# Performance work log

Hardware: AMD Instinct MI355X
Metric: run time of the kernel (lower is better)

The kernel has to match this reference:

```python
import jax, jax.numpy as jnp
import numpy as np

N_NODES = 8192
N_EDGES = 65536
D_MODEL = 64
D_INNER = 128
D_STATE = 16
DT_RANK = 4
LAYER_NUM = 3
TAU = 0.01


def _unif(key, shape, fan_out):
    stdv = 1.0 / np.sqrt(fan_out)
    return jax.random.uniform(key, shape, jnp.float32, -stdv, stdv)


def setup_inputs() -> dict:
    key = jax.random.key(0)
    ks = jax.random.split(key, 12)
    x = jax.random.normal(ks[0], (N_NODES, D_MODEL), jnp.float32)
    edge_index = jax.random.randint(ks[1], (2, N_EDGES), 0, N_NODES, jnp.int64)
    in_proj_w = _unif(ks[2], (D_MODEL, 2 * D_INNER), 2 * D_INNER)
    x_proj_w = _unif(ks[3], (D_INNER, DT_RANK + 2 * D_STATE), DT_RANK + 2 * D_STATE)
    dt_proj_w = _unif(ks[4], (DT_RANK, D_INNER), D_INNER)
    out_proj_w = _unif(ks[5], (D_INNER, D_MODEL), D_MODEL)
    A_log = jnp.log(jnp.broadcast_to(jnp.arange(1, D_STATE + 1, dtype=jnp.float32)[None, :], (D_INNER, D_STATE)))
    D = jnp.ones((D_INNER,), jnp.float32)
    in_act_w = _unif(ks[6], (D_INNER, 2), 2)
    in_act_b = _unif(ks[7], (2,), 2)
    out_act_w = _unif(ks[8], (D_INNER, 2), 2)
    out_act_b = _unif(ks[9], (2,), 2)
    return {"x": x, "in_proj_w": in_proj_w, "x_proj_w": x_proj_w, "dt_proj_w": dt_proj_w,
            "A_log": A_log, "D": D, "out_proj_w": out_proj_w,
            "in_act_w": in_act_w, "in_act_b": in_act_b, "out_act_w": out_act_w, "out_act_b": out_act_b,
            "edge_index": edge_index, "layer_num": LAYER_NUM}


def _norm_adj(row, col, w, n_nodes):
    # SparseTensor(...).set_diag() adds diag value 1; symmetric deg^-1/2 renorm
    deg = jax.ops.segment_sum(w, row, num_segments=n_nodes) + 1.0
    dinv = jnp.where(deg > 0, deg ** -0.5, 0.0)
    return dinv[row] * w * dinv[col], dinv * dinv  # off-diag edge weights, diag weights


def _spmm(row, col, ew, dw, x, n_nodes):
    # adj @ x with adj = edges(ew) + diag(dw); x: [N, F]
    return jax.ops.segment_sum(ew[:, None] * x[col], row, num_segments=n_nodes) + dw[:, None] * x


def _gumbel_hard(logits, key, tau):
    g = jax.random.gumbel(key, logits.shape, logits.dtype)
    y = jax.nn.softmax((logits + g) / tau, axis=-1)
    hard = jax.nn.one_hot(jnp.argmax(y, axis=-1), logits.shape[-1], dtype=y.dtype)
    return hard + y - jax.lax.stop_gradient(y)


def reference(x, in_proj_w, x_proj_w, dt_proj_w, A_log, D, out_proj_w,
              in_act_w, in_act_b, out_act_w, out_act_b, edge_index, layer_num):
    n_nodes, d_model = x.shape
    d_inner = dt_proj_w.shape[1]
    n = A_log.shape[1]
    dt_rank = dt_proj_w.shape[0]
    row, col = edge_index[0], edge_index[1]

    xl = jnp.broadcast_to(x[:, None, :], (n_nodes, layer_num, d_model))  # [N,L,d_model]
    x_and_res = xl @ in_proj_w                                           # [N,L,2*d_inner]
    xs, res = jnp.split(x_and_res, 2, axis=-1)
    xs = jax.nn.relu(xs)                                                 # u in scan

    A = -jnp.exp(A_log)                                                  # [d_inner, n]
    x_dbl = xs @ x_proj_w                                                # [N,L,dt_rank+2n]
    delta = jax.nn.softplus(x_dbl[..., :dt_rank] @ dt_proj_w)            # [N,L,d_inner]
    B = x_dbl[..., dt_rank:dt_rank + n]                                  # [N,L,n]
    C = x_dbl[..., dt_rank + n:]                                         # [N,L,n]

    deltaA = jnp.exp(jnp.einsum('bld,dn->bldn', delta, A))               # [N,L,d_inner,n]
    deltaB_u = jnp.einsum('bld,bln->bldn', delta * xs, B)                # [N,L,d_inner,n]

    # initial adjacency: unit-weight edges, sym-normalized with self loops
    ew, dw = _norm_adj(row, col, jnp.ones((row.shape[0],), xs.dtype), n_nodes)
    state = jnp.zeros((n_nodes, d_inner, n), xs.dtype)
    gkey = jax.random.key(42)
    ys = []
    for i in range(layer_num):  # small fixed number of GCN/SSM steps
        state = deltaA[:, i] * state + deltaB_u[:, i]
        y = jnp.einsum('bdn,bn->bd', state, C[:, i])                     # [N,d_inner]
        flat = _spmm(row, col, ew, dw, state.reshape(n_nodes, d_inner * n), n_nodes)
        state = flat.reshape(n_nodes, d_inner, n)
        in_p = _gumbel_hard(y @ in_act_w + in_act_b, jax.random.fold_in(gkey, 2 * i), TAU)
        out_p = _gumbel_hard(y @ out_act_w + out_act_b, jax.random.fold_in(gkey, 2 * i + 1), TAU)
        w = in_p[col, 0] * out_p[row, 0]  # keep_in_prob[v] * keep_out_prob[u]
        ew, dw = _norm_adj(row, col, w, n_nodes)
        ys.append(y)

    y = jnp.stack(ys, axis=1) + xs * D                                   # [N,L,d_inner]
    y = y * jax.nn.relu(res)
    out = y @ out_proj_w                                                 # [N,L,d_model]
    return out[:, -1, :]
```

## Files before the change

kernel.cpp:

```cpp
#include <hip/hip_runtime.h>
#include <cstdint>

#define NN 8192
#define NE 65536
#define G 8
#define CAP 64

typedef _Float16 h8 __attribute__((ext_vector_type(8)));
typedef _Float16 h2 __attribute__((ext_vector_type(2)));

__device__ inline int rdlane_i(int v, int l) {
  return __builtin_amdgcn_readlane(v, l);
}
__device__ inline float rdlane_f(float v, int l) {
  return __int_as_float(__builtin_amdgcn_readlane(__float_as_int(v), l));
}

__host__ __device__ inline void tf2x32(uint32_t k0, uint32_t k1,
                                       uint32_t x0, uint32_t x1,
                                       uint32_t& r0, uint32_t& r1) {
  uint32_t ks2 = k0 ^ k1 ^ 0x1BD11BDAu;
  x0 += k0; x1 += k1;
#define TF_ROT(x,d) (((x)<<(d))|((x)>>(32-(d))))
#define TF_R4(ra,rb,rc,rd) \
  x0+=x1; x1=TF_ROT(x1,ra); x1^=x0; \
  x0+=x1; x1=TF_ROT(x1,rb); x1^=x0; \
  x0+=x1; x1=TF_ROT(x1,rc); x1^=x0; \
  x0+=x1; x1=TF_ROT(x1,rd); x1^=x0;
  TF_R4(13,15,26,6)  x0+=k1;  x1+=ks2+1u;
  TF_R4(17,29,16,24) x0+=ks2; x1+=k0+2u;
  TF_R4(13,15,26,6)  x0+=k0;  x1+=k1+3u;
  TF_R4(17,29,16,24) x0+=k1;  x1+=ks2+4u;
  TF_R4(13,15,26,6)  x0+=ks2; x1+=k0+5u;
  r0=x0; r1=x1;
#undef TF_R4
#undef TF_ROT
}

__device__ inline float gumbel32(uint32_t k0, uint32_t k1, uint32_t idx) {
  uint32_t a, b;
  tf2x32(k0, k1, 0u, idx, a, b);
  uint32_t bits = a ^ b;
  float f = __uint_as_float((bits >> 9) | 0x3f800000u) - 1.0f;
  float u = (f > 0.0f) ? f : 1.17549435e-38f;
  return -logf(-logf(u));
}

__global__ __launch_bounds__(256) void k_nodeprep(
    const float* __restrict__ x, const float* __restrict__ ipw,
    const float* __restrict__ xpw, const float* __restrict__ dtw,
    const float* __restrict__ iaw, const float* __restrict__ iab,
    const float* __restrict__ oaw, const float* __restrict__ oab,
    const float* __restrict__ alog, const float* __restrict__ wout,
    const int* __restrict__ ei,
    uint32_t ki0, uint32_t ki1, uint32_t ko0, uint32_t ko1,
    float* __restrict__ xs, float* __restrict__ rres,
    float* __restrict__ delta, _Float16* __restrict__ dxh2,
    float* __restrict__ Bm, float* __restrict__ Cm,
    float* __restrict__ inp, float* __restrict__ outp,
    float* __restrict__ Amat, _Float16* __restrict__ woT,
    int* __restrict__ cnt, int* __restrict__ csr_col) {
  __shared__ float sxs[G][128];
  __shared__ float sdbl[G][36];
  __shared__ float sdx[G][128];
  int t = threadIdx.x;
  int b0 = blockIdx.x * G;
  if (t < 64) {
    int e = blockIdx.x * 64 + t;
    int v = ei[e];
    int pos = atomicAdd(&cnt[v], 1);
    if (pos < CAP) csr_col[(v<<6) + pos] = ei[NE + e];
  }
  {
    int i = blockIdx.x * 8 + (t & 7);
    if (t < 8) {
      int d = i >> 6, oc = i & 63;
      woT[oc*128 + d] = (_Float16)wout[i];
    }
  }
  if (blockIdx.x == 0) {
    for (int i = t; i < 2048; i += 256) Amat[i] = -expf(alog[i]);
  }
  float acc[G];
#pragma unroll
  for (int g = 0; g < G; g++) acc[g] = 0.f;
  const float4* xb = (const float4*)(x + (size_t)b0 * 64);
  for (int k4 = 0; k4 < 16; k4++) {
    float w0 = ipw[(k4*4+0)*256 + t];
    float w1 = ipw[(k4*4+1)*256 + t];
    float w2 = ipw[(k4*4+2)*256 + t];
    float w3 = ipw[(k4*4+3)*256 + t];
#pragma unroll
    for (int g = 0; g < G; g++) {
      float4 xv = xb[g*16 + k4];
      acc[g] += xv.x*w0; acc[g] += xv.y*w1; acc[g] += xv.z*w2; acc[g] += xv.w*w3;
    }
  }
  if (t < 128) {
#pragma unroll
    for (int g = 0; g < G; g++) {
      float v = fmaxf(acc[g], 0.f);
      sxs[g][t] = v;
      xs[(size_t)(b0+g)*128 + t] = v;
    }
  } else {
    int j = t - 128;
#pragma unroll
    for (int g = 0; g < G; g++) rres[(size_t)(b0+g)*128 + j] = fmaxf(acc[g], 0.f);
  }
  __syncthreads();
  for (int idx = t; idx < G*36; idx += 256) {
    int g = idx / 36, c = idx % 36;
    float a = 0.f;
    for (int d4 = 0; d4 < 32; d4++) {
      float4 sv = ((const float4*)&sxs[g][0])[d4];
      a += sv.x*xpw[(d4*4+0)*36 + c];
      a += sv.y*xpw[(d4*4+1)*36 + c];
      a += sv.z*xpw[(d4*4+2)*36 + c];
      a += sv.w*xpw[(d4*4+3)*36 + c];
    }
    sdbl[g][c] = a;
    if (c >= 4 && c < 20)  Bm[(b0+g)*16 + (c-4)]  = a;
    else if (c >= 20)      Cm[(b0+g)*16 + (c-20)] = a;
  }
  __syncthreads();
  {
    int d = t & 127, hi = t >> 7;
#pragma unroll
    for (int gg = 0; gg < G/2; gg++) {
      int g = hi*(G/2) + gg;
      int b = b0 + g;
      float dt = sdbl[g][0]*dtw[d]     + sdbl[g][1]*dtw[128+d]
               + sdbl[g][2]*dtw[256+d] + sdbl[g][3]*dtw[384+d];
      float dv = fmaxf(dt, 0.f) + log1pf(expf(-fabsf(dt)));
      delta[(size_t)b*128 + d] = dv;
      sdx[g][d] = dv * sxs[g][d];
    }
  }
  __syncthreads();
  for (int i = t; i < G*64; i += 256) {
    int g = i >> 6, d = i & 63;
    h2 pk;
    pk.x = (_Float16)sdx[g][d];
    pk.y = (_Float16)sdx[g][d + 64];
    ((h2*)(dxh2 + ((size_t)(b0+g) << 7)))[d] = pk;
  }
  int wid = t >> 6, lane = t & 63;
#pragma unroll
  for (int s = 0; s < 2; s++) {
    int g = wid*2 + s;
    int b = b0 + g;
    float da = sdx[g][lane], db = sdx[g][lane + 64];
    float4 pr;
    pr.x = da*iaw[2*lane]   + db*iaw[2*(lane+64)];
    pr.y = da*iaw[2*lane+1] + db*iaw[2*(lane+64)+1];
    pr.z = da*oaw[2*lane]   + db*oaw[2*(lane+64)];
    pr.w = da*oaw[2*lane+1] + db*oaw[2*(lane+64)+1];
    for (int off = 32; off >= 1; off >>= 1) {
      pr.x += __shfl_down(pr.x, off);
      pr.y += __shfl_down(pr.y, off);
      pr.z += __shfl_down(pr.z, off);
      pr.w += __shfl_down(pr.w, off);
    }
    float gsel = 0.f;
    if (lane < 4) {
      uint32_t kk0 = (lane < 2) ? ki0 : ko0;
      uint32_t kk1 = (lane < 2) ? ki1 : ko1;
      gsel = gumbel32(kk0, kk1, 2u*(uint32_t)b + (uint32_t)(lane & 1));
    }
    float g0 = __shfl(gsel, 0), g1 = __shfl(gsel, 1);
    float g2 = __shfl(gsel, 2), g3 = __shfl(gsel, 3);
    if (lane == 0) {
      float BC = 0.f;
      for (int n = 0; n < 16; n++) BC += sdbl[g][4+n] * sdbl[g][20+n];
      float li0 = BC*pr.x + iab[0], li1 = BC*pr.y + iab[1];
      float lo0 = BC*pr.z + oab[0], lo1 = BC*pr.w + oab[1];
      inp[b]  = (li0 + g0 >= li1 + g1) ? 1.0f : 0.0f;
      outp[b] = (lo0 + g2 >= lo1 + g3) ? 1.0f : 0.0f;
    }
  }
}

__global__ __launch_bounds__(256) void k_spmm0f(
    const int* __restrict__ cnt, const int* __restrict__ csr_col,
    const float* __restrict__ inp, const float* __restrict__ outp,
    const float* __restrict__ delta, const _Float16* __restrict__ dxh2,
    const float* __restrict__ Bm, const float* __restrict__ Cm,
    const float* __restrict__ Amat,
    _Float16* __restrict__ s_out, float* __restrict__ dinv1,
    float* __restrict__ y2p) {
  int t = threadIdx.x, wid = t >> 6, lane = t & 63;
  int v = (blockIdx.x << 2) + wid;
  int deg = min(cnt[v], CAP);
  int   creg = 0;
  float cfreg = 0.f, gl = 0.f;
  if (lane < deg) {
    creg = csr_col[(v << 6) + lane];
    cfreg = 1.0f / sqrtf((float)min(cnt[creg], CAP) + 1.0f);
    gl = inp[creg];
  }
  float degs = gl;
#pragma unroll
  for (int off = 32; off >= 1; off >>= 1) degs += __shfl_xor(degs, off);
  int d0 = lane, d1 = lane + 64;
  float dv = 1.0f / sqrtf((float)deg + 1.0f);
  h2 pkv = ((const h2*)(dxh2 + ((size_t)v << 7)))[d0];
  float dx0 = (float)pkv.x, dx1 = (float)pkv.y;
  float Bf[16];
  {
    const float4* p = (const float4*)(Bm + ((size_t)v << 4));
    float4 q0 = p[0], q1 = p[1], q2 = p[2], q3 = p[3];
    Bf[0]=q0.x; Bf[1]=q0.y; Bf[2]=q0.z; Bf[3]=q0.w;
    Bf[4]=q1.x; Bf[5]=q1.y; Bf[6]=q1.z; Bf[7]=q1.w;
    Bf[8]=q2.x; Bf[9]=q2.y; Bf[10]=q2.z; Bf[11]=q2.w;
    Bf[12]=q3.x; Bf[13]=q3.y; Bf[14]=q3.z; Bf[15]=q3.w;
  }
  float a0[16], a1[16];
  {
    float dw = dv * dv;
    float c0 = dw * dx0, c1 = dw * dx1;
#pragma unroll
    for (int n = 0; n < 16; n++) { a0[n] = c0*Bf[n]; a1[n] = c1*Bf[n]; }
  }
#pragma unroll 2
  for (int j = 0; j < deg; j++) {
    int   c  = rdlane_i(creg, j);
    float cf = rdlane_f(cfreg, j);
    float coef = dv * cf;
    h2 pk = ((const h2*)(dxh2 + ((size_t)c << 7)))[d0];
    const float4* bp = (const float4*)(Bm + ((size_t)c << 4));
    float4 B0 = bp[0], B1 = bp[1], B2 = bp[2], B3 = bp[3];
    float e0 = coef * (float)pk.x;
    float e1 = coef * (float)pk.y;
    a0[0]+=e0*B0.x; a0[1]+=e0*B0.y; a0[2]+=e0*B0.z; a0[3]+=e0*B0.w;
    a0[4]+=e0*B1.x; a0[5]+=e0*B1.y; a0[6]+=e0*B1.z; a0[7]+=e0*B1.w;
    a0[8]+=e0*B2.x; a0[9]+=e0*B2.y; a0[10]+=e0*B2.z; a0[11]+=e0*B2.w;
    a0[12]+=e0*B3.x; a0[13]+=e0*B3.y; a0[14]+=e0*B3.z; a0[15]+=e0*B3.w;
    a1[0]+=e1*B0.x; a1[1]+=e1*B0.y; a1[2]+=e1*B0.z; a1[3]+=e1*B0.w;
    a1[4]+=e1*B1.x; a1[5]+=e1*B1.y; a1[6]+=e1*B1.z; a1[7]+=e1*B1.w;
    a1[8]+=e1*B2.x; a1[9]+=e1*B2.y; a1[10]+=e1*B2.z; a1[11]+=e1*B2.w;
    a1[12]+=e1*B3.x; a1[13]+=e1*B3.y; a1[14]+=e1*B3.z; a1[15]+=e1*B3.w;
  }
  float de0 = delta[(size_t)v*128 + d0], de1 = delta[(size_t)v*128 + d1];
  const float4* A0p = (const float4*)(Amat + (d0 << 4));
  const float4* A1p = (const float4*)(Amat + (d1 << 4));
  const float4* Cp  = (const float4*)(Cm + ((size_t)v << 4));
  float d1v = 1.0f / sqrtf(outp[v]*degs + 1.0f);
  if (lane == 0) dinv1[v] = d1v;
  float dw1 = d1v * d1v;
  float y0 = 0.f, y1 = 0.f, BvC = 0.f;
  _Float16 sh0[16], sh1[16];
#pragma unroll
  for (int q = 0; q < 4; q++) {
    float4 Aq0 = A0p[q], Aq1 = A1p[q], Cq = Cp[q];
    float A0a[4] = {Aq0.x, Aq0.y, Aq0.z, Aq0.w};
    float A1a[4] = {Aq1.x, Aq1.y, Aq1.z, Aq1.w};
    float Ca[4]  = {Cq.x, Cq.y, Cq.z, Cq.w};
#pragma unroll
    for (int i = 0; i < 4; i++) {
      int n = 4*q + i;
      float E0 = expf(de0 * A0a[i]);
      float E1 = expf(de1 * A1a[i]);
      float s0 = E0*a0[n] + dx0*Bf[n];
      float s1 = E1*a1[n] + dx1*Bf[n];
      y0 += E0*s0*Ca[i];
      y1 += E1*s1*Ca[i];
      BvC += Bf[n]*Ca[i];
      sh0[n] = (_Float16)s0;
      sh1[n] = (_Float16)s1;
    }
  }
  y0 = dw1*y0 + dx0*BvC;
  y1 = dw1*y1 + dx1*BvC;
  if (inp[v] != 0.f) {
    h8 P00, P01, P10, P11;
#pragma unroll
    for (int i = 0; i < 8; i++) {
      P00[i] = sh0[i]; P01[i] = sh0[8+i];
      P10[i] = sh1[i]; P11[i] = sh1[8+i];
    }
    h8* op = (h8*)(s_out + ((size_t)v << 11));
    op[2*lane]           = P00;
    op[2*lane + 1]       = P01;
    op[128 + 2*lane]     = P10;
    op[128 + 2*lane + 1] = P11;
  }
  y2p[(size_t)v*128 + d0] = y0;
  y2p[(size_t)v*128 + d1] = y1;
}

__global__ __launch_bounds__(256) void k_spmm1fo(
    const int* __restrict__ cnt, const int* __restrict__ csr_col,
    const float* __restrict__ dinv1,
    const float* __restrict__ inp, const float* __restrict__ outp,
    const float* __restrict__ delta,
    const float* __restrict__ Cm, const float* __restrict__ Amat,
    const _Float16* __restrict__ s_in, const float* __restrict__ y2p,
    const float* __restrict__ xs, const float* __restrict__ rres,
    const float* __restrict__ Dv, const _Float16* __restrict__ woT,
    float* __restrict__ out) {
  __shared__ float ty[4][128];
  int t = threadIdx.x, wid = t >> 6, lane = t & 63;
  int v = (blockIdx.x << 2) + wid;
  int deg = (outp[v] != 0.f) ? min(cnt[v], CAP) : 0;
  int   creg = 0;
  float cfreg = 0.f;
  if (lane < deg) {
    creg = csr_col[(v << 6) + lane];
    float g = inp[creg];
    cfreg = (g != 0.f) ? dinv1[creg] : 0.f;
  }
  unsigned long long mask = __ballot(cfreg != 0.f);
  int d0 = lane, d1 = lane + 64;
  float y0 = 0.f, y1 = 0.f;
  if (mask != 0ull) {
    float dv = dinv1[v];
    float a0[16], a1[16];
#pragma unroll
    for (int n = 0; n < 16; n++) { a0[n] = 0.f; a1[n] = 0.f; }
#pragma unroll 2
    for (int j = 0; j < deg; j++) {
      float cf = rdlane_f(cfreg, j);
      if (cf == 0.f) continue;
      int c = rdlane_i(creg, j);
      float coef = dv * cf;
      const h8* rp = (const h8*)(s_in + ((size_t)c << 11));
      h8 n00 = rp[2*lane], n01 = rp[2*lane+1];
      h8 n10 = rp[128 + 2*lane], n11 = rp[128 + 2*lane+1];
      a0[0]+=coef*(float)n00[0]; a0[1]+=coef*(float)n00[1];
      a0[2]+=coef*(float)n00[2]; a0[3]+=coef*(float)n00[3];
      a0[4]+=coef*(float)n00[4]; a0[5]+=coef*(float)n00[5];
      a0[6]+=coef*(float)n00[6]; a0[7]+=coef*(float)n00[7];
      a0[8]+=coef*(float)n01[0]; a0[9]+=coef*(float)n01[1];
      a0[10]+=coef*(float)n01[2]; a0[11]+=coef*(float)n01[3];
      a0[12]+=coef*(float)n01[4]; a0[13]+=coef*(float)n01[5];
      a0[14]+=coef*(float)n01[6]; a0[15]+=coef*(float)n01[7];
      a1[0]+=coef*(float)n10[0]; a1[1]+=coef*(float)n10[1];
      a1[2]+=coef*(float)n10[2]; a1[3]+=coef*(float)n10[3];
      a1[4]+=coef*(float)n10[4]; a1[5]+=coef*(float)n10[5];
      a1[6]+=coef*(float)n10[6]; a1[7]+=coef*(float)n10[7];
      a1[8]+=coef*(float)n11[0]; a1[9]+=coef*(float)n11[1];
      a1[10]+=coef*(float)n11[2]; a1[11]+=coef*(float)n11[3];
      a1[12]+=coef*(float)n11[4]; a1[13]+=coef*(float)n11[5];
      a1[14]+=coef*(float)n11[6]; a1[15]+=coef*(float)n11[7];
    }
    float de0 = delta[(size_t)v*128 + d0], de1 = delta[(size_t)v*128 + d1];
    const float4* A0p = (const float4*)(Amat + (d0 << 4));
    const float4* A1p = (const float4*)(Amat + (d1 << 4));
    const float4* Cp  = (const float4*)(Cm + ((size_t)v << 4));
#pragma unroll
    for (int q = 0; q < 4; q++) {
      float4 Aq0 = A0p[q], Aq1 = A1p[q], Cq = Cp[q];
      float A0a[4] = {Aq0.x, Aq0.y, Aq0.z, Aq0.w};
      float A1a[4] = {Aq1.x, Aq1.y, Aq1.z, Aq1.w};
      float Ca[4]  = {Cq.x, Cq.y, Cq.z, Cq.w};
#pragma unroll
      for (int i = 0; i < 4; i++) {
        int n = 4*q + i;
        y0 += expf(de0*A0a[i]) * a0[n] * Ca[i];
        y1 += expf(de1*A1a[i]) * a1[n] * Ca[i];
      }
    }
  }
  float t0 = (y0 + y2p[(size_t)v*128 + d0] + xs[(size_t)v*128 + d0]*Dv[d0]) * rres[(size_t)v*128 + d0];
  float t1 = (y1 + y2p[(size_t)v*128 + d1] + xs[(size_t)v*128 + d1]*Dv[d1]) * rres[(size_t)v*128 + d1];
  ty[wid][d0] = t0;
  ty[wid][d1] = t1;
  asm volatile("s_waitcnt lgkmcnt(0)" ::: "memory");
  __builtin_amdgcn_sched_barrier(0);
  float acc = 0.f;
  const float4* tyv = (const float4*)&ty[wid][0];
  const h8* wrow = (const h8*)(woT + ((size_t)lane << 7));
#pragma unroll
  for (int ch = 0; ch < 16; ch++) {
    h8 wv = wrow[ch];
    float4 u0 = tyv[2*ch], u1 = tyv[2*ch+1];
    acc += u0.x*(float)wv[0] + u0.y*(float)wv[1] + u0.z*(float)wv[2] + u0.w*(float)wv[3]
         + u1.x*(float)wv[4] + u1.y*(float)wv[5] + u1.z*(float)wv[6] + u1.w*(float)wv[7];
  }
  out[(size_t)v*64 + lane] = acc;
}

extern "C" void kernel_launch(void* const* d_in, const int* in_sizes, int n_in,
                              void* d_out, int out_size, void* d_ws, size_t ws_size,
                              hipStream_t stream) {
  const float* x    = (const float*)d_in[0];
  const float* ipw  = (const float*)d_in[1];
  const float* xpw  = (const float*)d_in[2];
  const float* dtw  = (const float*)d_in[3];
  const float* alog = (const float*)d_in[4];
  const float* Dv   = (const float*)d_in[5];
  const float* wout = (const float*)d_in[6];
  const float* iaw  = (const float*)d_in[7];
  const float* iab  = (const float*)d_in[8];
  const float* oaw  = (const float*)d_in[9];
  const float* oab  = (const float*)d_in[10];
  const int*   ei   = (const int*)d_in[11];
  (void)in_sizes; (void)n_in; (void)out_size; (void)ws_size;

  float* W = (float*)d_ws;
  size_t o = 0;
  float* xs    = W + o; o += (size_t)NN*128;
  float* rres  = W + o; o += (size_t)NN*128;
  float* delta = W + o; o += (size_t)NN*128;
  float* y2p   = W + o; o += (size_t)NN*128;
  float* Bm    = W + o; o += (size_t)NN*16;
  float* Cm    = W + o; o += (size_t)NN*16;
  float* Amat  = W + o; o += 2048;
  float* dinv1 = W + o; o += NN;
  float* inp   = W + o; o += NN;
  float* outp  = W + o; o += NN;
  _Float16* dxh2 = (_Float16*)(W + o); o += (size_t)NN*64;
  o += (size_t)NN*8;
  _Float16* woT  = (_Float16*)(W + o); o += 4096;
  _Float16* stA  = (_Float16*)(W + o); o += (size_t)NN*1024;
  int* cnt     = (int*)(W + o);
  int* csr_col = cnt + NN;

  uint32_t ki0, ki1, ko0, ko1;
  tf2x32(0u, 42u, 0u, 0u, ki0, ki1);
  tf2x32(0u, 42u, 0u, 1u, ko0, ko1);

  hipMemsetAsync(cnt, 0, NN*sizeof(int), stream);

  k_nodeprep<<<NN/G, 256, 0, stream>>>(x, ipw, xpw, dtw, iaw, iab, oaw, oab,
                                       alog, wout, ei, ki0, ki1, ko0, ko1,
                                       xs, rres, delta, dxh2, Bm, Cm,
                                       inp, outp, Amat, woT, cnt, csr_col);

  k_spmm0f<<<NN/4, 256, 0, stream>>>(cnt, csr_col, inp, outp,
                                     delta, dxh2, Bm, Cm, Amat,
                                     stA, dinv1, y2p);

  k_spmm1fo<<<NN/4, 256, 0, stream>>>(cnt, csr_col, dinv1, inp, outp,
                                      delta, Cm, Amat, stA, y2p,
                                      xs, rres, Dv, woT, (float*)d_out);
}
```

Baseline: 160.3 us.

## Fuse three kernels into one persistent kernel with grid barriers

Merges the node-prep, first SpMM and second SpMM+output kernels into one persistent kernel of 512 blocks. Each block loops over its share of the work, and atomic spin-wait grid barriers separate the phases. The goal is to remove kernel launch gaps and inter-kernel drain and fill costs. In exchange, all 512 blocks must be co-resident on the GPU, parallelism per phase is lower than with the earlier grids, and the barriers cost spinning on atomics.

```diff
diff --git a/kernel.cpp b/kernel.cpp
--- a/kernel.cpp
+++ b/kernel.cpp
@@ -5,6 +5,7 @@
 #define NE 65536
 #define G 8
 #define CAP 64
+#define NB 512
 
 typedef _Float16 h8 __attribute__((ext_vector_type(8)));
 typedef _Float16 h2 __attribute__((ext_vector_type(2)));
@@ -14,6 +15,18 @@
 }
 __device__ inline float rdlane_f(float v, int l) {
   return __int_as_float(__builtin_amdgcn_readlane(__float_as_int(v), l));
+}
+
+__device__ inline void grid_bar(int* bar, int idx) {
+  __syncthreads();
+  if (threadIdx.x == 0) {
+    __hip_atomic_fetch_add(&bar[idx], 1, __ATOMIC_ACQ_REL, __HIP_MEMORY_SCOPE_AGENT);
+    long spins = 0;
+    while (__hip_atomic_load(&bar[idx], __ATOMIC_ACQUIRE, __HIP_MEMORY_SCOPE_AGENT) < NB
+           && spins < (1L << 28)) spins++;
+  }
+  __syncthreads();
+  __threadfence();
 }
 
 __host__ __device__ inline void tf2x32(uint32_t k0, uint32_t k1,
@@ -46,339 +59,338 @@
   return -logf(-logf(u));
 }
 
-__global__ __launch_bounds__(256) void k_nodeprep(
-    const float* __restrict__ x, const float* __restrict__ ipw,
-    const float* __restrict__ xpw, const float* __restrict__ dtw,
-    const float* __restrict__ iaw, const float* __restrict__ iab,
-    const float* __restrict__ oaw, const float* __restrict__ oab,
-    const float* __restrict__ alog, const float* __restrict__ wout,
-    const int* __restrict__ ei,
-    uint32_t ki0, uint32_t ki1, uint32_t ko0, uint32_t ko1,
-    float* __restrict__ xs, float* __restrict__ rres,
-    float* __restrict__ delta, _Float16* __restrict__ dxh2,
-    float* __restrict__ Bm, float* __restrict__ Cm,
-    float* __restrict__ inp, float* __restrict__ outp,
-    float* __restrict__ Amat, _Float16* __restrict__ woT,
-    int* __restrict__ cnt, int* __restrict__ csr_col) {
+struct KArgs {
+  const float *x, *ipw, *xpw, *dtw, *iaw, *iab, *oaw, *oab, *alog, *wout;
+  const int* ei;
+  uint32_t ki0, ki1, ko0, ko1;
+  float *xs, *rres, *delta;
+  _Float16 *dxh2;
+  float *Bm, *Cm, *inp, *outp, *Amat;
+  _Float16 *woT;
+  int *cnt, *csr_col, *bar;
+  _Float16 *stA;
+  float *dinv1, *y2p;
+  const float *Dv;
+  float *out;
+};
+
+__global__ __launch_bounds__(256, 2) void k_fused(KArgs A) {
+  int t = threadIdx.x;
+  int bid = blockIdx.x;
   __shared__ float sxs[G][128];
   __shared__ float sdbl[G][36];
   __shared__ float sdx[G][128];
-  int t = threadIdx.x;
-  int b0 = blockIdx.x * G;
-  if (t < 64) {
-    int e = blockIdx.x * 64 + t;
-    int v = ei[e];
-    int pos = atomicAdd(&cnt[v], 1);
-    if (pos < CAP) csr_col[(v<<6) + pos] = ei[NE + e];
+  __shared__ float sty[4][128];
+
+  if (bid == 0) {
+    for (int i = t; i < 2048; i += 256) A.Amat[i] = -expf(A.alog[i]);
   }
+  for (int p = bid; p < NN/G; p += NB) {
+    int b0 = p * G;
+    if (t < 64) {
+      int e = p * 64 + t;
+      int v = A.ei[e];
+      int pos = atomicAdd(&A.cnt[v], 1);
+      if (pos < CAP) A.csr_col[(v<<6) + pos] = A.ei[NE + e];
+    }
+    {
+      int i = p * 8 + (t & 7);
+      if (t < 8) {
+        int d = i >> 6, oc = i & 63;
+        A.woT[oc*128 + d] = (_Float16)A.wout[i];
+      }
+    }
+    float acc[G];
+#pragma unroll
+    for (int g = 0; g < G; g++) acc[g] = 0.f;
+    const float4* xb = (const float4*)(A.x + (size_t)b0 * 64);
+    for (int k4 = 0; k4 < 16; k4++) {
+      float w0 = A.ipw[(k4*4+0)*256 + t];
+      float w1 = A.ipw[(k4*4+1)*256 + t];
+      float w2 = A.ipw[(k4*4+2)*256 + t];
+      float w3 = A.ipw[(k4*4+3)*256 + t];
+#pragma unroll
+      for (int g = 0; g < G; g++) {
+        float4 xv = xb[g*16 + k4];
+        acc[g] += xv.x*w0; acc[g] += xv.y*w1; acc[g] += xv.z*w2; acc[g] += xv.w*w3;
+      }
+    }
+    if (t < 128) {
+#pragma unroll
+      for (int g = 0; g < G; g++) {
+        float v = fmaxf(acc[g], 0.f);
+        sxs[g][t] = v;
+        A.xs[(size_t)(b0+g)*128 + t] = v;
+      }
+    } else {
+      int j = t - 128;
+#pragma unroll
+      for (int g = 0; g < G; g++) A.rres[(size_t)(b0+g)*128 + j] = fmaxf(acc[g], 0.f);
+    }
+    __syncthreads();
+    for (int idx = t; idx < G*36; idx += 256) {
+      int g = idx / 36, c = idx % 36;
+      float a = 0.f;
+      for (int d4 = 0; d4 < 32; d4++) {
+        float4 sv = ((const float4*)&sxs[g][0])[d4];
+        a += sv.x*A.xpw[(d4*4+0)*36 + c];
+        a += sv.y*A.xpw[(d4*4+1)*36 + c];
+        a += sv.z*A.xpw[(d4*4+2)*36 + c];
+        a += sv.w*A.xpw[(d4*4+3)*36 + c];
+      }
+      sdbl[g][c] = a;
+      if (c >= 4 && c < 20)  A.Bm[(b0+g)*16 + (c-4)]  = a;
+      else if (c >= 20)      A.Cm[(b0+g)*16 + (c-20)] = a;
+    }
+    __syncthreads();
+    {
+      int d = t & 127, hi = t >> 7;
+#pragma unroll
+      for (int gg = 0; gg < G/2; gg++) {
+        int g = hi*(G/2) + gg;
+        int b = b0 + g;
+        float dt = sdbl[g][0]*A.dtw[d]     + sdbl[g][1]*A.dtw[128+d]
+                 + sdbl[g][2]*A.dtw[256+d] + sdbl[g][3]*A.dtw[384+d];
+        float dv = fmaxf(dt, 0.f) + log1pf(expf(-fabsf(dt)));
+        A.delta[(size_t)b*128 + d] = dv;
+        sdx[g][d] = dv * sxs[g][d];
+      }
+    }
+    __syncthreads();
+    for (int i = t; i < G*64; i += 256) {
+      int g = i >> 6, d = i & 63;
+      h2 pk;
+      pk.x = (_Float16)sdx[g][d];
+      pk.y = (_Float16)sdx[g][d + 64];
+      ((h2*)(A.dxh2 + ((size_t)(b0+g) << 7)))[d] = pk;
+    }
+    int wid = t >> 6, lane = t & 63;
+#pragma unroll
+    for (int s = 0; s < 2; s++) {
+      int g = wid*2 + s;
+      int b = b0 + g;
+      float da = sdx[g][lane], db = sdx[g][lane + 64];
+      float4 pr;
+      pr.x = da*A.iaw[2*lane]   + db*A.iaw[2*(lane+64)];
+      pr.y = da*A.iaw[2*lane+1] + db*A.iaw[2*(lane+64)+1];
+      pr.z = da*A.oaw[2*lane]   + db*A.oaw[2*(lane+64)];
+      pr.w = da*A.oaw[2*lane+1] + db*A.oaw[2*(lane+64)+1];
+      for (int off = 32; off >= 1; off >>= 1) {
+        pr.x += __shfl_down(pr.x, off);
+        pr.y += __shfl_down(pr.y, off);
+        pr.z += __shfl_down(pr.z, off);
+        pr.w += __shfl_down(pr.w, off);
+      }
+      float gsel = 0.f;
+      if (lane < 4) {
+        uint32_t kk0 = (lane < 2) ? A.ki0 : A.ko0;
+        uint32_t kk1 = (lane < 2) ? A.ki1 : A.ko1;
+        gsel = gumbel32(kk0, kk1, 2u*(uint32_t)b + (uint32_t)(lane & 1));
+      }
+      float g0 = __shfl(gsel, 0), g1 = __shfl(gsel, 1);
+      float g2 = __shfl(gsel, 2), g3 = __shfl(gsel, 3);
+      if (lane == 0) {
+        float BC = 0.f;
+        for (int n = 0; n < 16; n++) BC += sdbl[g][4+n] * sdbl[g][20+n];
+        float li0 = BC*pr.x + A.iab[0], li1 = BC*pr.y + A.iab[1];
+        float lo0 = BC*pr.z + A.oab[0], lo1 = BC*pr.w + A.oab[1];
+        A.inp[b]  = (li0 + g0 >= li1 + g1) ? 1.0f : 0.0f;
+        A.outp[b] = (lo0 + g2 >= lo1 + g3) ? 1.0f : 0.0f;
+      }
+    }
+    __syncthreads();
+  }
+
+  grid_bar(A.bar, 0);
+
   {
-    int i = blockIdx.x * 8 + (t & 7);
-    if (t < 8) {
-      int d = i >> 6, oc = i & 63;
-      woT[oc*128 + d] = (_Float16)wout[i];
+    int wid = t >> 6, lane = t & 63;
+    for (int u = bid; u < NN/4; u += NB) {
+      int v = (u << 2) + wid;
+      int deg = min(A.cnt[v], CAP);
+      int   creg = 0;
+      float cfreg = 0.f, gl = 0.f;
+      if (lane < deg) {
+        creg = A.csr_col[(v << 6) + lane];
+        cfreg = 1.0f / sqrtf((float)min(A.cnt[creg], CAP) + 1.0f);
+        gl = A.inp[creg];
+      }
+      float degs = gl;
+#pragma unroll
+      for (int off = 32; off >= 1; off >>= 1) degs += __shfl_xor(degs, off);
+      int d0 = lane, d1 = lane + 64;
+      float dv = 1.0f / sqrtf((float)deg + 1.0f);
+      h2 pkv = ((const h2*)(A.dxh2 + ((size_t)v << 7)))[d0];
+      float dx0 = (float)pkv.x, dx1 = (float)pkv.y;
+      float Bf[16];
+      {
+        const float4* p = (const float4*)(A.Bm + ((size_t)v << 4));
+        float4 q0 = p[0], q1 = p[1], q2 = p[2], q3 = p[3];
+        Bf[0]=q0.x; Bf[1]=q0.y; Bf[2]=q0.z; Bf[3]=q0.w;
+        Bf[4]=q1.x; Bf[5]=q1.y; Bf[6]=q1.z; Bf[7]=q1.w;
+        Bf[8]=q2.x; Bf[9]=q2.y; Bf[10]=q2.z; Bf[11]=q2.w;
+        Bf[12]=q3.x; Bf[13]=q3.y; Bf[14]=q3.z; Bf[15]=q3.w;
+      }
+      float a0[16], a1[16];
+      {
+        float dw = dv * dv;
+        float c0 = dw * dx0, c1 = dw * dx1;
+#pragma unroll
+        for (int n = 0; n < 16; n++) { a0[n] = c0*Bf[n]; a1[n] = c1*Bf[n]; }
+      }
+#pragma unroll 2
+      for (int j = 0; j < deg; j++) {
+        int   c  = rdlane_i(creg, j);
+        float cf = rdlane_f(cfreg, j);
+        float coef = dv * cf;
+        h2 pk = ((const h2*)(A.dxh2 + ((size_t)c << 7)))[d0];
+        const float4* bp = (const float4*)(A.Bm + ((size_t)c << 4));
+        float4 B0 = bp[0], B1 = bp[1], B2 = bp[2], B3 = bp[3];
+        float e0 = coef * (float)pk.x;
+        float e1 = coef * (float)pk.y;
+        a0[0]+=e0*B0.x; a0[1]+=e0*B0.y; a0[2]+=e0*B0.z; a0[3]+=e0*B0.w;
+        a0[4]+=e0*B1.x; a0[5]+=e0*B1.y; a0[6]+=e0*B1.z; a0[7]+=e0*B1.w;
+        a0[8]+=e0*B2.x; a0[9]+=e0*B2.y; a0[10]+=e0*B2.z; a0[11]+=e0*B2.w;
+        a0[12]+=e0*B3.x; a0[13]+=e0*B3.y; a0[14]+=e0*B3.z; a0[15]+=e0*B3.w;
+        a1[0]+=e1*B0.x; a1[1]+=e1*B0.y; a1[2]+=e1*B0.z; a1[3]+=e1*B0.w;
+        a1[4]+=e1*B1.x; a1[5]+=e1*B1.y; a1[6]+=e1*B1.z; a1[7]+=e1*B1.w;
+        a1[8]+=e1*B2.x; a1[9]+=e1*B2.y; a1[10]+=e1*B2.z; a1[11]+=e1*B2.w;
+        a1[12]+=e1*B3.x; a1[13]+=e1*B3.y; a1[14]+=e1*B3.z; a1[15]+=e1*B3.w;
+      }
+      float de0 = A.delta[(size_t)v*128 + d0], de1 = A.delta[(size_t)v*128 + d1];
+      const float4* A0p = (const float4*)(A.Amat + (d0 << 4));
+      const float4* A1p = (const float4*)(A.Amat + (d1 << 4));
+      const float4* Cp  = (const float4*)(A.Cm + ((size_t)v << 4));
+      float d1v = 1.0f / sqrtf(A.outp[v]*degs + 1.0f);
+      if (lane == 0) A.dinv1[v] = d1v;
+      float dw1 = d1v * d1v;
+      float y0 = 0.f, y1 = 0.f, BvC = 0.f;
+      _Float16 sh0[16], sh1[16];
+#pragma unroll
+      for (int q = 0; q < 4; q++) {
+        float4 Aq0 = A0p[q], Aq1 = A1p[q], Cq = Cp[q];
+        float A0a[4] = {Aq0.x, Aq0.y, Aq0.z, Aq0.w};
+        float A1a[4] = {Aq1.x, Aq1.y, Aq1.z, Aq1.w};
+        float Ca[4]  = {Cq.x, Cq.y, Cq.z, Cq.w};
+#pragma unroll
+        for (int i = 0; i < 4; i++) {
+          int n = 4*q + i;
+          float E0 = expf(de0 * A0a[i]);
+          float E1 = expf(de1 * A1a[i]);
+          float s0 = E0*a0[n] + dx0*Bf[n];
+          float s1 = E1*a1[n] + dx1*Bf[n];
+          y0 += E0*s0*Ca[i];
+          y1 += E1*s1*Ca[i];
+          BvC += Bf[n]*Ca[i];
+          sh0[n] = (_Float16)s0;
+          sh1[n] = (_Float16)s1;
+        }
+      }
+      y0 = dw1*y0 + dx0*BvC;
+      y1 = dw1*y1 + dx1*BvC;
+      if (A.inp[v] != 0.f) {
+        h8 P00, P01, P10, P11;
+#pragma unroll
+        for (int i = 0; i < 8; i++) {
+          P00[i] = sh0[i]; P01[i] = sh0[8+i];
+          P10[i] = sh1[i]; P11[i] = sh1[8+i];
+        }
+        h8* op = (h8*)(A.stA + ((size_t)v << 11));
+        op[2*lane]           = P00;
+        op[2*lane + 1]       = P01;
+        op[128 + 2*lane]     = P10;
+        op[128 + 2*lane + 1] = P11;
+      }
+      A.y2p[(size_t)v*128 + d0] = y0;
+      A.y2p[(size_t)v*128 + d1] = y1;
     }
   }
-  if (blockIdx.x == 0) {
-    for (int i = t; i < 2048; i += 256) Amat[i] = -expf(alog[i]);
+
+  grid_bar(A.bar, 1);
+
+  {
+    int wid = t >> 6, lane = t & 63;
+    for (int u = bid; u < NN/4; u += NB) {
+      int v = (u << 2) + wid;
+      int deg = (A.outp[v] != 0.f) ? min(A.cnt[v], CAP) : 0;
+      int   creg = 0;
+      float cfreg = 0.f;
+      if (lane < deg) {
+        creg = A.csr_col[(v << 6) + lane];
+        float g = A.inp[creg];
+        cfreg = (g != 0.f) ? A.dinv1[creg] : 0.f;
+      }
+      unsigned long long mask = __ballot(cfreg != 0.f);
+      int d0 = lane, d1 = lane + 64;
+      float y0 = 0.f, y1 = 0.f;
+      if (mask != 0ull) {
+        float dv = A.dinv1[v];
+        float a0[16], a1[16];
+#pragma unroll
+        for (int n = 0; n < 16; n++) { a0[n] = 0.f; a1[n] = 0.f; }
+#pragma unroll 2
+        for (int j = 0; j < deg; j++) {
+          float cf = rdlane_f(cfreg, j);
+          if (cf == 0.f) continue;
+          int c = rdlane_i(creg, j);
+          float coef = dv * cf;
+          const h8* rp = (const h8*)(A.stA + ((size_t)c << 11));
+          h8 n00 = rp[2*lane], n01 = rp[2*lane+1];
+          h8 n10 = rp[128 + 2*lane], n11 = rp[128 + 2*lane+1];
+          a0[0]+=coef*(float)n00[0]; a0[1]+=coef*(float)n00[1];
+          a0[2]+=coef*(float)n00[2]; a0[3]+=coef*(float)n00[3];
+          a0[4]+=coef*(float)n00[4]; a0[5]+=coef*(float)n00[5];
+          a0[6]+=coef*(float)n00[6]; a0[7]+=coef*(float)n00[7];
+          a0[8]+=coef*(float)n01[0]; a0[9]+=coef*(float)n01[1];
+          a0[10]+=coef*(float)n01[2]; a0[11]+=coef*(float)n01[3];
+          a0[12]+=coef*(float)n01[4]; a0[13]+=coef*(float)n01[5];
+          a0[14]+=coef*(float)n01[6]; a0[15]+=coef*(float)n01[7];
+          a1[0]+=coef*(float)n10[0]; a1[1]+=coef*(float)n10[1];
+          a1[2]+=coef*(float)n10[2]; a1[3]+=coef*(float)n10[3];
+          a1[4]+=coef*(float)n10[4]; a1[5]+=coef*(float)n10[5];
+          a1[6]+=coef*(float)n10[6]; a1[7]+=coef*(float)n10[7];
+          a1[8]+=coef*(float)n11[0]; a1[9]+=coef*(float)n11[1];
+          a1[10]+=coef*(float)n11[2]; a1[11]+=coef*(float)n11[3];
+          a1[12]+=coef*(float)n11[4]; a1[13]+=coef*(float)n11[5];
+          a1[14]+=coef*(float)n11[6]; a1[15]+=coef*(float)n11[7];
+        }
+        float de0 = A.delta[(size_t)v*128 + d0], de1 = A.delta[(size_t)v*128 + d1];
+        const float4* A0p = (const float4*)(A.Amat + (d0 << 4));
+        const float4* A1p = (const float4*)(A.Amat + (d1 << 4));
+        const float4* Cp  = (const float4*)(A.Cm + ((size_t)v << 4));
+#pragma unroll
+        for (int q = 0; q < 4; q++) {
+          float4 Aq0 = A0p[q], Aq1 = A1p[q], Cq = Cp[q];
+          float A0a[4] = {Aq0.x, Aq0.y, Aq0.z, Aq0.w};
+          float A1a[4] = {Aq1.x, Aq1.y, Aq1.z, Aq1.w};
+          float Ca[4]  = {Cq.x, Cq.y, Cq.z, Cq.w};
+#pragma unroll
+          for (int i = 0; i < 4; i++) {
+            int n = 4*q + i;
+            y0 += expf(de0*A0a[i]) * a0[n] * Ca[i];
+            y1 += expf(de1*A1a[i]) * a1[n] * Ca[i];
+          }
+        }
+      }
+      float t0 = (y0 + A.y2p[(size_t)v*128 + d0] + A.xs[(size_t)v*128 + d0]*A.Dv[d0]) * A.rres[(size_t)v*128 + d0];
+      float t1 = (y1 + A.y2p[(size_t)v*128 + d1] + A.xs[(size_t)v*128 + d1]*A.Dv[d1]) * A.rres[(size_t)v*128 + d1];
+      sty[wid][d0] = t0;
+      sty[wid][d1] = t1;
+      asm volatile("s_waitcnt lgkmcnt(0)" ::: "memory");
+      __builtin_amdgcn_sched_barrier(0);
+      float acc = 0.f;
+      const float4* tyv = (const float4*)&sty[wid][0];
+      const h8* wrow = (const h8*)(A.woT + ((size_t)lane << 7));
+#pragma unroll
+      for (int ch = 0; ch < 16; ch++) {
+        h8 wv = wrow[ch];
+        float4 u0 = tyv[2*ch], u1 = tyv[2*ch+1];
+        acc += u0.x*(float)wv[0] + u0.y*(float)wv[1] + u0.z*(float)wv[2] + u0.w*(float)wv[3]
+             + u1.x*(float)wv[4] + u1.y*(float)wv[5] + u1.z*(float)wv[6] + u1.w*(float)wv[7];
+      }
+      A.out[(size_t)v*64 + lane] = acc;
+    }
   }
-  float acc[G];
-#pragma unroll
-  for (int g = 0; g < G; g++) acc[g] = 0.f;
-  const float4* xb = (const float4*)(x + (size_t)b0 * 64);
-  for (int k4 = 0; k4 < 16; k4++) {
-    float w0 = ipw[(k4*4+0)*256 + t];
-    float w1 = ipw[(k4*4+1)*256 + t];
-    float w2 = ipw[(k4*4+2)*256 + t];
-    float w3 = ipw[(k4*4+3)*256 + t];
-#pragma unroll
-    for (int g = 0; g < G; g++) {
-      float4 xv = xb[g*16 + k4];
-      acc[g] += xv.x*w0; acc[g] += xv.y*w1; acc[g] += xv.z*w2; acc[g] += xv.w*w3;
-    }
-  }
-  if (t < 128) {
-#pragma unroll
-    for (int g = 0; g < G; g++) {
-      float v = fmaxf(acc[g], 0.f);
-      sxs[g][t] = v;
-      xs[(size_t)(b0+g)*128 + t] = v;
-    }
-  } else {
-    int j = t - 128;
-#pragma unroll
-    for (int g = 0; g < G; g++) rres[(size_t)(b0+g)*128 + j] = fmaxf(acc[g], 0.f);
-  }
-  __syncthreads();
-  for (int idx = t; idx < G*36; idx += 256) {
-    int g = idx / 36, c = idx % 36;
-    float a = 0.f;
-    for (int d4 = 0; d4 < 32; d4++) {
-      float4 sv = ((const float4*)&sxs[g][0])[d4];
-      a += sv.x*xpw[(d4*4+0)*36 + c];
-      a += sv.y*xpw[(d4*4+1)*36 + c];
-      a += sv.z*xpw[(d4*4+2)*36 + c];
-      a += sv.w*xpw[(d4*4+3)*36 + c];
-    }
-    sdbl[g][c] = a;
-    if (c >= 4 && c < 20)  Bm[(b0+g)*16 + (c-4)]  = a;
-    else if (c >= 20)      Cm[(b0+g)*16 + (c-20)] = a;
-  }
-  __syncthreads();
-  {
-    int d = t & 127, hi = t >> 7;
-#pragma unroll
-    for (int gg = 0; gg < G/2; gg++) {
-      int g = hi*(G/2) + gg;
-      int b = b0 + g;
-      float dt = sdbl[g][0]*dtw[d]     + sdbl[g][1]*dtw[128+d]
-               + sdbl[g][2]*dtw[256+d] + sdbl[g][3]*dtw[384+d];
-      float dv = fmaxf(dt, 0.f) + log1pf(expf(-fabsf(dt)));
-      delta[(size_t)b*128 + d] = dv;
-      sdx[g][d] = dv * sxs[g][d];
-    }
-  }
-  __syncthreads();
-  for (int i = t; i < G*64; i += 256) {
-    int g = i >> 6, d = i & 63;
-    h2 pk;
-    pk.x = (_Float16)sdx[g][d];
-    pk.y = (_Float16)sdx[g][d + 64];
-    ((h2*)(dxh2 + ((size_t)(b0+g) << 7)))[d] = pk;
-  }
-  int wid = t >> 6, lane = t & 63;
-#pragma unroll
-  for (int s = 0; s < 2; s++) {
-    int g = wid*2 + s;
-    int b = b0 + g;
-    float da = sdx[g][lane], db = sdx[g][lane + 64];
-    float4 pr;
-    pr.x = da*iaw[2*lane]   + db*iaw[2*(lane+64)];
-    pr.y = da*iaw[2*lane+1] + db*iaw[2*(lane+64)+1];
-    pr.z = da*oaw[2*lane]   + db*oaw[2*(lane+64)];
-    pr.w = da*oaw[2*lane+1] + db*oaw[2*(lane+64)+1];
-    for (int off = 32; off >= 1; off >>= 1) {
-      pr.x += __shfl_down(pr.x, off);
-      pr.y += __shfl_down(pr.y, off);
-      pr.z += __shfl_down(pr.z, off);
-      pr.w += __shfl_down(pr.w, off);
-    }
-    float gsel = 0.f;
-    if (lane < 4) {
-      uint32_t kk0 = (lane < 2) ? ki0 : ko0;
-      uint32_t kk1 = (lane < 2) ? ki1 : ko1;
-      gsel = gumbel32(kk0, kk1, 2u*(uint32_t)b + (uint32_t)(lane & 1));
-    }
-    float g0 = __shfl(gsel, 0), g1 = __shfl(gsel, 1);
-    float g2 = __shfl(gsel, 2), g3 = __shfl(gsel, 3);
-    if (lane == 0) {
-      float BC = 0.f;
-      for (int n = 0; n < 16; n++) BC += sdbl[g][4+n] * sdbl[g][20+n];
-      float li0 = BC*pr.x + iab[0], li1 = BC*pr.y + iab[1];
-      float lo0 = BC*pr.z + oab[0], lo1 = BC*pr.w + oab[1];
-      inp[b]  = (li0 + g0 >= li1 + g1) ? 1.0f : 0.0f;
-      outp[b] = (lo0 + g2 >= lo1 + g3) ? 1.0f : 0.0f;
-    }
-  }
-}
-
-__global__ __launch_bounds__(256) void k_spmm0f(
-    const int* __restrict__ cnt, const int* __restrict__ csr_col,
-    const float* __restrict__ inp, const float* __restrict__ outp,
-    const float* __restrict__ delta, const _Float16* __restrict__ dxh2,
-    const float* __restrict__ Bm, const float* __restrict__ Cm,
-    const float* __restrict__ Amat,
-    _Float16* __restrict__ s_out, float* __restrict__ dinv1,
-    float* __restrict__ y2p) {
-  int t = threadIdx.x, wid = t >> 6, lane = t & 63;
-  int v = (blockIdx.x << 2) + wid;
-  int deg = min(cnt[v], CAP);
-  int   creg = 0;
-  float cfreg = 0.f, gl = 0.f;
-  if (lane < deg) {
-    creg = csr_col[(v << 6) + lane];
-    cfreg = 1.0f / sqrtf((float)min(cnt[creg], CAP) + 1.0f);
-    gl = inp[creg];
-  }
-  float degs = gl;
-#pragma unroll
-  for (int off = 32; off >= 1; off >>= 1) degs += __shfl_xor(degs, off);
-  int d0 = lane, d1 = lane + 64;
-  float dv = 1.0f / sqrtf((float)deg + 1.0f);
-  h2 pkv = ((const h2*)(dxh2 + ((size_t)v << 7)))[d0];
-  float dx0 = (float)pkv.x, dx1 = (float)pkv.y;
-  float Bf[16];
-  {
-    const float4* p = (const float4*)(Bm + ((size_t)v << 4));
-    float4 q0 = p[0], q1 = p[1], q2 = p[2], q3 = p[3];
-    Bf[0]=q0.x; Bf[1]=q0.y; Bf[2]=q0.z; Bf[3]=q0.w;
-    Bf[4]=q1.x; Bf[5]=q1.y; Bf[6]=q1.z; Bf[7]=q1.w;
-    Bf[8]=q2.x; Bf[9]=q2.y; Bf[10]=q2.z; Bf[11]=q2.w;
-    Bf[12]=q3.x; Bf[13]=q3.y; Bf[14]=q3.z; Bf[15]=q3.w;
-  }
-  float a0[16], a1[16];
-  {
-    float dw = dv * dv;
-    float c0 = dw * dx0, c1 = dw * dx1;
-#pragma unroll
-    for (int n = 0; n < 16; n++) { a0[n] = c0*Bf[n]; a1[n] = c1*Bf[n]; }
-  }
-#pragma unroll 2
-  for (int j = 0; j < deg; j++) {
-    int   c  = rdlane_i(creg, j);
-    float cf = rdlane_f(cfreg, j);
-    float coef = dv * cf;
-    h2 pk = ((const h2*)(dxh2 + ((size_t)c << 7)))[d0];
-    const float4* bp = (const float4*)(Bm + ((size_t)c << 4));
-    float4 B0 = bp[0], B1 = bp[1], B2 = bp[2], B3 = bp[3];
-    float e0 = coef * (float)pk.x;
-    float e1 = coef * (float)pk.y;
-    a0[0]+=e0*B0.x; a0[1]+=e0*B0.y; a0[2]+=e0*B0.z; a0[3]+=e0*B0.w;
-    a0[4]+=e0*B1.x; a0[5]+=e0*B1.y; a0[6]+=e0*B1.z; a0[7]+=e0*B1.w;
-    a0[8]+=e0*B2.x; a0[9]+=e0*B2.y; a0[10]+=e0*B2.z; a0[11]+=e0*B2.w;
-    a0[12]+=e0*B3.x; a0[13]+=e0*B3.y; a0[14]+=e0*B3.z; a0[15]+=e0*B3.w;
-    a1[0]+=e1*B0.x; a1[1]+=e1*B0.y; a1[2]+=e1*B0.z; a1[3]+=e1*B0.w;
-    a1[4]+=e1*B1.x; a1[5]+=e1*B1.y; a1[6]+=e1*B1.z; a1[7]+=e1*B1.w;
-    a1[8]+=e1*B2.x; a1[9]+=e1*B2.y; a1[10]+=e1*B2.z; a1[11]+=e1*B2.w;
-    a1[12]+=e1*B3.x; a1[13]+=e1*B3.y; a1[14]+=e1*B3.z; a1[15]+=e1*B3.w;
-  }
-  float de0 = delta[(size_t)v*128 + d0], de1 = delta[(size_t)v*128 + d1];
-  const float4* A0p = (const float4*)(Amat + (d0 << 4));
-  const float4* A1p = (const float4*)(Amat + (d1 << 4));
-  const float4* Cp  = (const float4*)(Cm + ((size_t)v << 4));
-  float d1v = 1.0f / sqrtf(outp[v]*degs + 1.0f);
-  if (lane == 0) dinv1[v] = d1v;
-  float dw1 = d1v * d1v;
-  float y0 = 0.f, y1 = 0.f, BvC = 0.f;
-  _Float16 sh0[16], sh1[16];
-#pragma unroll
-  for (int q = 0; q < 4; q++) {
-    float4 Aq0 = A0p[q], Aq1 = A1p[q], Cq = Cp[q];
-    float A0a[4] = {Aq0.x, Aq0.y, Aq0.z, Aq0.w};
-    float A1a[4] = {Aq1.x, Aq1.y, Aq1.z, Aq1.w};
-    float Ca[4]  = {Cq.x, Cq.y, Cq.z, Cq.w};
-#pragma unroll
-    for (int i = 0; i < 4; i++) {
-      int n = 4*q + i;
-      float E0 = expf(de0 * A0a[i]);
-      float E1 = expf(de1 * A1a[i]);
-      float s0 = E0*a0[n] + dx0*Bf[n];
-      float s1 = E1*a1[n] + dx1*Bf[n];
-      y0 += E0*s0*Ca[i];
-      y1 += E1*s1*Ca[i];
-      BvC += Bf[n]*Ca[i];
-      sh0[n] = (_Float16)s0;
-      sh1[n] = (_Float16)s1;
-    }
-  }
-  y0 = dw1*y0 + dx0*BvC;
-  y1 = dw1*y1 + dx1*BvC;
-  if (inp[v] != 0.f) {
-    h8 P00, P01, P10, P11;
-#pragma unroll
-    for (int i = 0; i < 8; i++) {
-      P00[i] = sh0[i]; P01[i] = sh0[8+i];
-      P10[i] = sh1[i]; P11[i] = sh1[8+i];
-    }
-    h8* op = (h8*)(s_out + ((size_t)v << 11));
-    op[2*lane]           = P00;
-    op[2*lane + 1]       = P01;
-    op[128 + 2*lane]     = P10;
-    op[128 + 2*lane + 1] = P11;
-  }
-  y2p[(size_t)v*128 + d0] = y0;
-  y2p[(size_t)v*128 + d1] = y1;
-}
-
-__global__ __launch_bounds__(256) void k_spmm1fo(
-    const int* __restrict__ cnt, const int* __restrict__ csr_col,
-    const float* __restrict__ dinv1,
-    const float* __restrict__ inp, const float* __restrict__ outp,
-    const float* __restrict__ delta,
-    const float* __restrict__ Cm, const float* __restrict__ Amat,
-    const _Float16* __restrict__ s_in, const float* __restrict__ y2p,
-    const float* __restrict__ xs, const float* __restrict__ rres,
-    const float* __restrict__ Dv, const _Float16* __restrict__ woT,
-    float* __restrict__ out) {
-  __shared__ float ty[4][128];
-  int t = threadIdx.x, wid = t >> 6, lane = t & 63;
-  int v = (blockIdx.x << 2) + wid;
-  int deg = (outp[v] != 0.f) ? min(cnt[v], CAP) : 0;
-  int   creg = 0;
-  float cfreg = 0.f;
-  if (lane < deg) {
-    creg = csr_col[(v << 6) + lane];
-    float g = inp[creg];
-    cfreg = (g != 0.f) ? dinv1[creg] : 0.f;
-  }
-  unsigned long long mask = __ballot(cfreg != 0.f);
-  int d0 = lane, d1 = lane + 64;
-  float y0 = 0.f, y1 = 0.f;
-  if (mask != 0ull) {
-    float dv = dinv1[v];
-    float a0[16], a1[16];
-#pragma unroll
-    for (int n = 0; n < 16; n++) { a0[n] = 0.f; a1[n] = 0.f; }
-#pragma unroll 2
-    for (int j = 0; j < deg; j++) {
-      float cf = rdlane_f(cfreg, j);
-      if (cf == 0.f) continue;
-      int c = rdlane_i(creg, j);
-      float coef = dv * cf;
-      const h8* rp = (const h8*)(s_in + ((size_t)c << 11));
-      h8 n00 = rp[2*lane], n01 = rp[2*lane+1];
-      h8 n10 = rp[128 + 2*lane], n11 = rp[128 + 2*lane+1];
-      a0[0]+=coef*(float)n00[0]; a0[1]+=coef*(float)n00[1];
-      a0[2]+=coef*(float)n00[2]; a0[3]+=coef*(float)n00[3];
-      a0[4]+=coef*(float)n00[4]; a0[5]+=coef*(float)n00[5];
-      a0[6]+=coef*(float)n00[6]; a0[7]+=coef*(float)n00[7];
-      a0[8]+=coef*(float)n01[0]; a0[9]+=coef*(float)n01[1];
-      a0[10]+=coef*(float)n01[2]; a0[11]+=coef*(float)n01[3];
-      a0[12]+=coef*(float)n01[4]; a0[13]+=coef*(float)n01[5];
-      a0[14]+=coef*(float)n01[6]; a0[15]+=coef*(float)n01[7];
-      a1[0]+=coef*(float)n10[0]; a1[1]+=coef*(float)n10[1];
-      a1[2]+=coef*(float)n10[2]; a1[3]+=coef*(float)n10[3];
-      a1[4]+=coef*(float)n10[4]; a1[5]+=coef*(float)n10[5];
-      a1[6]+=coef*(float)n10[6]; a1[7]+=coef*(float)n10[7];
-      a1[8]+=coef*(float)n11[0]; a1[9]+=coef*(float)n11[1];
-      a1[10]+=coef*(float)n11[2]; a1[11]+=coef*(float)n11[3];
-      a1[12]+=coef*(float)n11[4]; a1[13]+=coef*(float)n11[5];
-      a1[14]+=coef*(float)n11[6]; a1[15]+=coef*(float)n11[7];
-    }
-    float de0 = delta[(size_t)v*128 + d0], de1 = delta[(size_t)v*128 + d1];
-    const float4* A0p = (const float4*)(Amat + (d0 << 4));
-    const float4* A1p = (const float4*)(Amat + (d1 << 4));
-    const float4* Cp  = (const float4*)(Cm + ((size_t)v << 4));
-#pragma unroll
-    for (int q = 0; q < 4; q++) {
-      float4 Aq0 = A0p[q], Aq1 = A1p[q], Cq = Cp[q];
-      float A0a[4] = {Aq0.x, Aq0.y, Aq0.z, Aq0.w};
-      float A1a[4] = {Aq1.x, Aq1.y, Aq1.z, Aq1.w};
-      float Ca[4]  = {Cq.x, Cq.y, Cq.z, Cq.w};
-#pragma unroll
-      for (int i = 0; i < 4; i++) {
-        int n = 4*q + i;
-        y0 += expf(de0*A0a[i]) * a0[n] * Ca[i];
-        y1 += expf(de1*A1a[i]) * a1[n] * Ca[i];
-      }
-    }
-  }
-  float t0 = (y0 + y2p[(size_t)v*128 + d0] + xs[(size_t)v*128 + d0]*Dv[d0]) * rres[(size_t)v*128 + d0];
-  float t1 = (y1 + y2p[(size_t)v*128 + d1] + xs[(size_t)v*128 + d1]*Dv[d1]) * rres[(size_t)v*128 + d1];
-  ty[wid][d0] = t0;
-  ty[wid][d1] = t1;
-  asm volatile("s_waitcnt lgkmcnt(0)" ::: "memory");
-  __builtin_amdgcn_sched_barrier(0);
-  float acc = 0.f;
-  const float4* tyv = (const float4*)&ty[wid][0];
-  const h8* wrow = (const h8*)(woT + ((size_t)lane << 7));
-#pragma unroll
-  for (int ch = 0; ch < 16; ch++) {
-    h8 wv = wrow[ch];
-    float4 u0 = tyv[2*ch], u1 = tyv[2*ch+1];
-    acc += u0.x*(float)wv[0] + u0.y*(float)wv[1] + u0.z*(float)wv[2] + u0.w*(float)wv[3]
-         + u1.x*(float)wv[4] + u1.y*(float)wv[5] + u1.z*(float)wv[6] + u1.w*(float)wv[7];
-  }
-  out[(size_t)v*64 + lane] = acc;
 }
 
 extern "C" void kernel_launch(void* const* d_in, const int* in_sizes, int n_in,
@@ -414,25 +426,26 @@
   o += (size_t)NN*8;
   _Float16* woT  = (_Float16*)(W + o); o += 4096;
   _Float16* stA  = (_Float16*)(W + o); o += (size_t)NN*1024;
-  int* cnt     = (int*)(W + o);
+  int* bar     = (int*)(W + o);
+  int* cnt     = bar + 4;
   int* csr_col = cnt + NN;
 
   uint32_t ki0, ki1, ko0, ko1;
   tf2x32(0u, 42u, 0u, 0u, ki0, ki1);
   tf2x32(0u, 42u, 0u, 1u, ko0, ko1);
 
-  hipMemsetAsync(cnt, 0, NN*sizeof(int), stream);
-
-  k_nodeprep<<<NN/G, 256, 0, stream>>>(x, ipw, xpw, dtw, iaw, iab, oaw, oab,
-                                       alog, wout, ei, ki0, ki1, ko0, ko1,
-                                       xs, rres, delta, dxh2, Bm, Cm,
-                                       inp, outp, Amat, woT, cnt, csr_col);
-
-  k_spmm0f<<<NN/4, 256, 0, stream>>>(cnt, csr_col, inp, outp,
-                                     delta, dxh2, Bm, Cm, Amat,
-                                     stA, dinv1, y2p);
-
-  k_spmm1fo<<<NN/4, 256, 0, stream>>>(cnt, csr_col, dinv1, inp, outp,
-                                      delta, Cm, Amat, stA, y2p,
-                                      xs, rres, Dv, woT, (float*)d_out);
-}
+  hipMemsetAsync(bar, 0, (4 + NN)*sizeof(int), stream);
+
+  KArgs A;
+  A.x = x; A.ipw = ipw; A.xpw = xpw; A.dtw = dtw;
+  A.iaw = iaw; A.iab = iab; A.oaw = oaw; A.oab = oab;
+  A.alog = alog; A.wout = wout; A.ei = ei;
+  A.ki0 = ki0; A.ki1 = ki1; A.ko0 = ko0; A.ko1 = ko1;
+  A.xs = xs; A.rres = rres; A.delta = delta; A.dxh2 = dxh2;
+  A.Bm = Bm; A.Cm = Cm; A.inp = inp; A.outp = outp; A.Amat = Amat;
+  A.woT = woT; A.cnt = cnt; A.csr_col = csr_col; A.bar = bar;
+  A.stA = stA; A.dinv1 = dinv1; A.y2p = y2p;
+  A.Dv = Dv; A.out = (float*)d_out;
+
+  k_fused<<<NB, 256, 0, stream>>>(A);
+}
```

After: 398.9 us. 149% more time.
